# Performance work log

Hardware: AMD Instinct MI355X
Metric: run time of the kernel (lower is better)

Reference implementation:

```python
import jax, jax.numpy as jnp
import numpy as np

B, T, C = 8, 1024, 1024
H, D = 16, 64  # num_heads, head_size

def setup_inputs() -> dict:
    key = jax.random.key(0)
    ks = jax.random.split(key, 6)
    s = C ** -0.5
    return {
        "x": jax.random.normal(ks[0], (B, T, C), dtype=jnp.float32),
        "Wq": jax.random.normal(ks[1], (H, C, D), dtype=jnp.float32) * s,
        "Wk": jax.random.normal(ks[2], (H, C, D), dtype=jnp.float32) * s,
        "Wv": jax.random.normal(ks[3], (H, C, D), dtype=jnp.float32) * s,
        "Wproj": jax.random.normal(ks[4], (H * D, C), dtype=jnp.float32) * ((H * D) ** -0.5),
        "bproj": jnp.zeros((C,), dtype=jnp.float32),
    }

def reference(x, Wq, Wk, Wv, Wproj, bproj):
    # per-head QKV projections, batched over heads via einsum (same math as looped heads)
    q = jnp.einsum('btc,hcd->bhtd', x, Wq)
    k = jnp.einsum('btc,hcd->bhtd', x, Wk)
    v = jnp.einsum('btc,hcd->bhtd', x, Wv)
    scale = D ** -0.5  # k.shape[-1]**-0.5 in original head
    scores = jnp.einsum('bhtd,bhsd->bhts', q, k) * scale  # [B,H,T,T]
    Tn = x.shape[1]
    causal = jnp.tril(jnp.ones((Tn, Tn), dtype=bool))
    scores = jnp.where(causal, scores, jnp.float32(-jnp.inf))
    att = jax.nn.softmax(scores, axis=-1)
    out = jnp.einsum('bhts,bhsd->bhtd', att, v)          # [B,H,T,D]
    out = out.transpose(0, 2, 1, 3).reshape(x.shape[0], Tn, H * D)  # concat heads
    return out @ Wproj + bproj  # dropout is identity at p=0.0
```

## Files before the change

### kernel.cpp

```cpp
#include <hip/hip_runtime.h>
#include <hip/hip_bf16.h>

#define B_ 8
#define T_ 1024
#define C_ 1024
#define H_ 16
#define D_ 64
#define QKVLD 3072

typedef short v4s __attribute__((ext_vector_type(4)));
typedef short v8s __attribute__((ext_vector_type(8)));
typedef float v4f __attribute__((ext_vector_type(4)));
typedef float v16f __attribute__((ext_vector_type(16)));

__device__ __forceinline__ unsigned short f2b(float f) {
    unsigned int u = __builtin_bit_cast(unsigned int, f);
    unsigned int lsb = (u >> 16) & 1u;
    u += 0x7fffu + lsb;
    return (unsigned short)(u >> 16);
}

__device__ __forceinline__ float fexp2(float x) {
    return __expf(x * 0.69314718056f);
}

__device__ __forceinline__ v4s pack4(float p0, float p1, float p2, float p3) {
    unsigned int a = (__builtin_bit_cast(unsigned int, p0) + 0x8000u) >> 16;
    unsigned int b = (__builtin_bit_cast(unsigned int, p1) + 0x8000u) & 0xFFFF0000u;
    unsigned int c = (__builtin_bit_cast(unsigned int, p2) + 0x8000u) >> 16;
    unsigned int d = (__builtin_bit_cast(unsigned int, p3) + 0x8000u) & 0xFFFF0000u;
    union { unsigned int u[2]; v4s v; } t;
    t.u[0] = a | b; t.u[1] = c | d;
    return t.v;
}

#define MFMA32(A, B, C) __builtin_amdgcn_mfma_f32_16x16x32_bf16(A, B, C, 0, 0, 0)
#define MFMA16(A, B, C) __builtin_amdgcn_mfma_f32_16x16x16bf16_1k(A, B, C, 0, 0, 0)

#define GLOAD16(gp, lp)                                                          \
    __builtin_amdgcn_global_load_lds(                                            \
        (const __attribute__((address_space(1))) unsigned int*)(gp),             \
        (__attribute__((address_space(3))) unsigned int*)(lp), 16, 0, 0)

__global__ void prep_kernel(const float* __restrict__ x, const float* __restrict__ Wq,
                            const float* __restrict__ Wk, const float* __restrict__ Wv,
                            const float* __restrict__ Wproj,
                            unsigned short* __restrict__ xb,
                            unsigned short* __restrict__ WqkvT,
                            unsigned short* __restrict__ WprojT) {
    __shared__ unsigned short t[64][65];
    int g = blockIdx.x;
    if (g < 8192) {
        int i = (g * 256 + (int)threadIdx.x) * 4;
        float4 v = *(const float4*)(x + i);
        ushort4 o;
        o.x = f2b(v.x); o.y = f2b(v.y); o.z = f2b(v.z); o.w = f2b(v.w);
        *(ushort4*)(xb + i) = o;
    } else if (g < 8192 + 768) {
        int idx = g - 8192;
        int z = idx >> 4;
        int h = z / 3, part = z % 3;
        const float* src = (part == 0 ? Wq : (part == 1 ? Wk : Wv)) + (size_t)h * C_ * D_;
        int c0 = (idx & 15) * 64;
        for (int i = threadIdx.x; i < 4096; i += 256) {
            int r = i >> 6, d = i & 63;
            t[d][r] = f2b(src[(size_t)(c0 + r) * D_ + d]);
        }
        __syncthreads();
        unsigned short* dst = WqkvT + (size_t)(h * 192 + part * 64) * C_;
        for (int i = threadIdx.x; i < 4096; i += 256) {
            int d = i >> 6, r = i & 63;
            dst[(size_t)d * C_ + c0 + r] = t[d][r];
        }
    } else {
        int idx = g - 8960;
        int n0 = (idx & 15) * 64, k0 = (idx >> 4) * 64;
        for (int i = threadIdx.x; i < 4096; i += 256) {
            int r = i >> 6, c = i & 63;
            t[c][r] = f2b(Wproj[(size_t)(k0 + r) * C_ + n0 + c]);
        }
        __syncthreads();
        for (int i = threadIdx.x; i < 4096; i += 256) {
            int n = i >> 6, k = i & 63;
            WprojT[(size_t)(n0 + n) * 1024 + k0 + k] = t[n][k];
        }
    }
}

__global__ __launch_bounds__(256, 2) void gemm_qkv(const unsigned short* __restrict__ A,
                                                   const unsigned short* __restrict__ Bt,
                                                   unsigned short* __restrict__ Cout,
                                                   int M, int N, int K) {
    __shared__ unsigned short lA[2][256 * 32];
    __shared__ unsigned short lB[2][128 * 32];
    int tid = threadIdx.x;
    int m0 = blockIdx.y * 256, n0 = blockIdx.x * 128;
    int lane = tid & 63, w = tid >> 6;
    int half = lane >> 5, l32 = lane & 31;
    int wm = w >> 1, wn = w & 1;

    const unsigned short* gA[4];
    int offA[4];
    #pragma unroll
    for (int j = 0; j < 4; j++) {
        int c = j * 256 + tid;
        int row = c >> 2;
        int col8 = ((c & 3) ^ ((row >> 1) & 3)) * 8;
        gA[j] = A + (size_t)(m0 + row) * K + col8;
        offA[j] = (j * 256 + w * 64) * 16;
    }
    const unsigned short* gB[2];
    int offB[2];
    #pragma unroll
    for (int j = 0; j < 2; j++) {
        int c = j * 256 + tid;
        int row = c >> 2;
        int col8 = ((c & 3) ^ ((row >> 1) & 3)) * 8;
        gB[j] = Bt + (size_t)(n0 + row) * K + col8;
        offB[j] = (j * 256 + w * 64) * 16;
    }

    int am[4], bn[2];
    #pragma unroll
    for (int mi = 0; mi < 4; mi++) am[mi] = wm * 128 + mi * 32 + l32;
    #pragma unroll
    for (int ni = 0; ni < 2; ni++) bn[ni] = wn * 64 + ni * 32 + l32;

    v16f acc[4][2];
    #pragma unroll
    for (int mi = 0; mi < 4; mi++)
        #pragma unroll
        for (int ni = 0; ni < 2; ni++)
            #pragma unroll
            for (int r = 0; r < 16; r++) acc[mi][ni][r] = 0.f;

    int ktiles = K >> 5;
    #pragma unroll
    for (int j = 0; j < 4; j++) GLOAD16(gA[j], (char*)&lA[0][0] + offA[j]);
    #pragma unroll
    for (int j = 0; j < 2; j++) GLOAD16(gB[j], (char*)&lB[0][0] + offB[j]);

    for (int it = 0; it < ktiles; it++) {
        int cur = it & 1, nxt = cur ^ 1;
        __asm__ volatile("s_waitcnt vmcnt(0)" ::: "memory");
        __asm__ volatile("s_barrier" ::: "memory");
        {
            int kn = (it + 1 < ktiles) ? (it + 1) * 32 : it * 32;
            #pragma unroll
            for (int j = 0; j < 4; j++) GLOAD16(gA[j] + kn, (char*)&lA[nxt][0] + offA[j]);
            #pragma unroll
            for (int j = 0; j < 2; j++) GLOAD16(gB[j] + kn, (char*)&lB[nxt][0] + offB[j]);
        }
        #pragma unroll
        for (int step = 0; step < 2; step++) {
            int g = step * 2 + half;
            v8s af[4], bf[2];
            #pragma unroll
            for (int mi = 0; mi < 4; mi++)
                af[mi] = *(const v8s*)&lA[cur][am[mi] * 32 + ((g ^ ((am[mi] >> 1) & 3)) * 8)];
            #pragma unroll
            for (int ni = 0; ni < 2; ni++)
                bf[ni] = *(const v8s*)&lB[cur][bn[ni] * 32 + ((g ^ ((bn[ni] >> 1) & 3)) * 8)];
            #pragma unroll
            for (int mi = 0; mi < 4; mi++)
                #pragma unroll
                for (int ni = 0; ni < 2; ni++)
                    acc[mi][ni] = __builtin_amdgcn_mfma_f32_32x32x16_bf16(af[mi], bf[ni], acc[mi][ni], 0, 0, 0);
        }
    }
    #pragma unroll
    for (int mi = 0; mi < 4; mi++) {
        #pragma unroll
        for (int ni = 0; ni < 2; ni++) {
            int col = n0 + wn * 64 + ni * 32 + l32;
            #pragma unroll
            for (int r = 0; r < 16; r++) {
                int row = m0 + wm * 128 + mi * 32 + (r & 3) + 8 * (r >> 2) + 4 * half;
                Cout[(size_t)row * N + col] = f2b(acc[mi][ni][r]);
            }
        }
    }
}

__global__ __launch_bounds__(256, 3) void gemm_proj(const unsigned short* __restrict__ A,
                                                    const unsigned short* __restrict__ Bt,
                                                    float* __restrict__ Cout,
                                                    const float* __restrict__ bias,
                                                    int M, int N, int K) {
    constexpr int ABUF = 128 * 32;
    constexpr int BBUF = 128 * 32;
    __shared__ unsigned short lA[3 * ABUF];
    __shared__ unsigned short lB[3 * BBUF];

    int tid = threadIdx.x;
    int lane = tid & 63, w = tid >> 6;
    int half = lane >> 5, l32 = lane & 31;
    int wm = w >> 1, wn = w & 1;

    int g = blockIdx.x;
    int nbm = M / 128;
    int stripe = nbm >> 3;
    int xcd = g & 7, s = g >> 3;
    int m0 = (xcd * stripe + (s % stripe)) * 128;
    int n0 = (s / stripe) * 128;

    const unsigned short* gA[2];
    int offA[2];
    #pragma unroll
    for (int j = 0; j < 2; j++) {
        int c = j * 256 + tid;
        int row = c >> 2;
        int col8 = ((c & 3) ^ ((row >> 1) & 3)) * 8;
        gA[j] = A + (size_t)(m0 + row) * K + col8;
        offA[j] = (j * 256 + w * 64) * 16;
    }
    const unsigned short* gB[2];
    int offB[2];
    #pragma unroll
    for (int j = 0; j < 2; j++) {
        int c = j * 256 + tid;
        int row = c >> 2;
        int col8 = ((c & 3) ^ ((row >> 1) & 3)) * 8;
        gB[j] = Bt + (size_t)(n0 + row) * K + col8;
        offB[j] = (j * 256 + w * 64) * 16;
    }

    int am[2], bn[2];
    #pragma unroll
    for (int mi = 0; mi < 2; mi++) am[mi] = wm * 64 + mi * 32 + l32;
    #pragma unroll
    for (int ni = 0; ni < 2; ni++) bn[ni] = wn * 64 + ni * 32 + l32;

    v16f acc[2][2];
    #pragma unroll
    for (int mi = 0; mi < 2; mi++)
        #pragma unroll
        for (int ni = 0; ni < 2; ni++)
            #pragma unroll
            for (int r = 0; r < 16; r++) acc[mi][ni][r] = 0.f;

    int kt = K >> 5;
    #pragma unroll
    for (int j = 0; j < 2; j++) GLOAD16(gA[j], (char*)lA + offA[j]);
    #pragma unroll
    for (int j = 0; j < 2; j++) GLOAD16(gB[j], (char*)lB + offB[j]);
    #pragma unroll
    for (int j = 0; j < 2; j++) GLOAD16(gA[j] + 32, (char*)(lA + ABUF) + offA[j]);
    #pragma unroll
    for (int j = 0; j < 2; j++) GLOAD16(gB[j] + 32, (char*)(lB + BBUF) + offB[j]);

    int cur = 0;
    for (int it = 0; it < kt; it++) {
        int nx2 = cur + 2; if (nx2 >= 3) nx2 -= 3;
        __asm__ volatile("s_waitcnt vmcnt(4)" ::: "memory");
        __asm__ volatile("s_barrier" ::: "memory");
        {
            int kn = ((it + 2 < kt) ? it + 2 : kt - 1) << 5;
            #pragma unroll
            for (int j = 0; j < 2; j++) GLOAD16(gA[j] + kn, (char*)(lA + nx2 * ABUF) + offA[j]);
            #pragma unroll
            for (int j = 0; j < 2; j++) GLOAD16(gB[j] + kn, (char*)(lB + nx2 * BBUF) + offB[j]);
        }
        const unsigned short* bufA = lA + cur * ABUF;
        const unsigned short* bufB = lB + cur * BBUF;
        #pragma unroll
        for (int step = 0; step < 2; step++) {
            int gch = step * 2 + half;
            v8s af[2], bf[2];
            #pragma unroll
            for (int mi = 0; mi < 2; mi++)
                af[mi] = *(const v8s*)&bufA[am[mi] * 32 + ((gch ^ ((am[mi] >> 1) & 3)) * 8)];
            #pragma unroll
            for (int ni = 0; ni < 2; ni++)
                bf[ni] = *(const v8s*)&bufB[bn[ni] * 32 + ((gch ^ ((bn[ni] >> 1) & 3)) * 8)];
            #pragma unroll
            for (int mi = 0; mi < 2; mi++)
                #pragma unroll
                for (int ni = 0; ni < 2; ni++)
                    acc[mi][ni] = __builtin_amdgcn_mfma_f32_32x32x16_bf16(af[mi], bf[ni], acc[mi][ni], 0, 0, 0);
        }
        cur = cur + 1; if (cur >= 3) cur -= 3;
    }
    #pragma unroll
    for (int mi = 0; mi < 2; mi++) {
        #pragma unroll
        for (int ni = 0; ni < 2; ni++) {
            int col = n0 + wn * 64 + ni * 32 + l32;
            #pragma unroll
            for (int r = 0; r < 16; r++) {
                int row = m0 + wm * 64 + mi * 32 + (r & 3) + 8 * (r >> 2) + 4 * half;
                Cout[(size_t)row * N + col] = acc[mi][ni][r] + bias[col];
            }
        }
    }
}

__global__ void transpose_v(const unsigned short* __restrict__ QKV, unsigned short* __restrict__ Vt) {
    int t0 = blockIdx.x * 64;
    int bh = blockIdx.y;
    int b = bh >> 4, h = bh & 15;
    __shared__ unsigned short t[64][65];
    for (int i = threadIdx.x; i < 4096; i += 256) {
        int r = i >> 6, d = i & 63;
        t[d][r] = QKV[(size_t)(b * T_ + t0 + r) * QKVLD + h * 192 + 128 + d];
    }
    __syncthreads();
    for (int i = threadIdx.x; i < 4096; i += 256) {
        int d = i >> 6, r = i & 63;
        Vt[((size_t)bh * 64 + d) * T_ + t0 + r] = t[d][r];
    }
}

__global__ __launch_bounds__(256) void attn_kernel(const unsigned short* __restrict__ QKV,
                                                   const unsigned short* __restrict__ Vt,
                                                   unsigned short* __restrict__ Ob) {
    int bh = blockIdx.x;
    int qt = 7 - blockIdx.y;
    int b = bh >> 4, h = bh & 15;
    int tid = threadIdx.x, lane = tid & 63, w = tid >> 6;
    int quad = lane >> 4, l16 = lane & 15;
    int qg0 = qt * 128 + w * 32;

    __shared__ unsigned short lK[2][2][64][32];
    __shared__ unsigned short lV[2][64][32];

    v8s aq[2][2];
    #pragma unroll
    for (int st = 0; st < 2; st++) {
        const unsigned short* qp = QKV + (size_t)(b * T_ + qg0 + st * 16 + l16) * QKVLD + h * 192;
        aq[st][0] = *(const v8s*)(qp + quad * 8);
        aq[st][1] = *(const v8s*)(qp + 32 + quad * 8);
    }

    const unsigned short* gK[2];
    const unsigned short* gV[2];
    int ldsOff[2];
    #pragma unroll
    for (int j = 0; j < 2; j++) {
        int c = j * 256 + tid;
        int halfp = c >> 8, row = (c >> 2) & 63;
        int col8 = ((c & 3) ^ ((row >> 1) & 3)) * 8;
        gK[j] = QKV + (size_t)(b * T_ + row) * QKVLD + h * 192 + 64 + halfp * 32 + col8;
        gV[j] = Vt + ((size_t)bh * 64 + row) * T_ + halfp * 32 + col8;
        ldsOff[j] = (j * 256 + w * 64) * 16;
    }
    int rcol = (quad ^ ((l16 >> 1) & 3)) * 8;

    v4f accO[2][4];
    float lsum[2] = {0.f, 0.f};
    #pragma unroll
    for (int st = 0; st < 2; st++)
        #pragma unroll
        for (int i = 0; i < 4; i++) accO[st][i] = (v4f){0.f, 0.f, 0.f, 0.f};

    int ntiles = 2 * qt + 2;
    const float SC = 0.1803368801f;

    #pragma unroll
    for (int j = 0; j < 2; j++)
        GLOAD16(gK[j], (char*)&lK[0][0][0][0] + ldsOff[j]);

    for (int it = 0; it < ntiles; it++) {
        int cur = it & 1, nxt = cur ^ 1;
        int s0 = it * 64;
        __asm__ volatile("s_waitcnt vmcnt(0)" ::: "memory");
        __asm__ volatile("s_barrier" ::: "memory");
        #pragma unroll
        for (int j = 0; j < 2; j++)
            GLOAD16(gV[j] + s0, (char*)&lV[0][0][0] + ldsOff[j]);
        __asm__ volatile("" ::: "memory");
        {
            int itn = (it + 1 < ntiles) ? it + 1 : it;
            size_t koff = (size_t)itn * 64 * QKVLD;
            #pragma unroll
            for (int j = 0; j < 2; j++)
                GLOAD16(gK[j] + koff, (char*)&lK[nxt][0][0][0] + ldsOff[j]);
        }
        bool act0 = (qg0 + 15 >= s0);
        bool act1 = (qg0 + 31 >= s0);
        v4s pP[2][4];
        if (act1) {
            v4f sf[2][4];
            #pragma unroll
            for (int nt = 0; nt < 4; nt++) {
                v8s bk0 = *(const v8s*)&lK[cur][0][nt * 16 + l16][rcol];
                v8s bk1 = *(const v8s*)&lK[cur][1][nt * 16 + l16][rcol];
                v4f a1 = (v4f){0.f, 0.f, 0.f, 0.f};
                a1 = MFMA32(bk0, aq[1][0], a1);
                a1 = MFMA32(bk1, aq[1][1], a1);
                sf[1][nt] = a1;
                if (act0) {
                    v4f a0 = (v4f){0.f, 0.f, 0.f, 0.f};
                    a0 = MFMA32(bk0, aq[0][0], a0);
                    a0 = MFMA32(bk1, aq[0][1], a0);
                    sf[0][nt] = a0;
                }
            }
            bool diag = (it >= ntiles - 2);
            #pragma unroll
            for (int st = 0; st < 2; st++) {
                if (st == 0 && !act0) continue;
                int qg = qg0 + st * 16 + l16;
                #pragma unroll
                for (int nt = 0; nt < 4; nt++) {
                    float p[4];
                    #pragma unroll
                    for (int r = 0; r < 4; r++) {
                        if (diag) {
                            int sg = s0 + nt * 16 + quad * 4 + r;
                            p[r] = (sg > qg) ? 0.f : fexp2(sf[st][nt][r] * SC);
                        } else {
                            p[r] = fexp2(sf[st][nt][r] * SC);
                        }
                        lsum[st] += p[r];
                    }
                    pP[st][nt] = pack4(p[0], p[1], p[2], p[3]);
                }
            }
        }
        __asm__ volatile("s_waitcnt vmcnt(2)" ::: "memory");
        __asm__ volatile("s_barrier" ::: "memory");
        if (act1) {
            #pragma unroll
            for (int kb = 0; kb < 4; kb++) {
                int sc_ = kb >> 1;
                int ccg = (kb & 1) * 2 + (quad >> 1);
                #pragma unroll
                for (int dt = 0; dt < 4; dt++) {
                    int d = dt * 16 + l16;
                    int ccp = ccg ^ ((l16 >> 1) & 3);
                    v4s bv = *(const v4s*)&lV[sc_][d][ccp * 8 + (quad & 1) * 4];
                    accO[1][dt] = MFMA16(pP[1][kb], bv, accO[1][dt]);
                    if (act0) accO[0][dt] = MFMA16(pP[0][kb], bv, accO[0][dt]);
                }
            }
        }
    }
    #pragma unroll
    for (int st = 0; st < 2; st++) {
        float ls = lsum[st];
        ls += __shfl_xor(ls, 16, 64);
        ls += __shfl_xor(ls, 32, 64);
        #pragma unroll
        for (int r = 0; r < 4; r++) {
            float lq = __shfl(ls, quad * 4 + r, 64);
            float inv = 1.0f / lq;
            int q = qg0 + st * 16 + quad * 4 + r;
            #pragma unroll
            for (int dt = 0; dt < 4; dt++) {
                int d = dt * 16 + l16;
                Ob[(size_t)(b * T_ + q) * (H_ * D_) + h * 64 + d] = f2b(accO[st][dt][r] * inv);
            }
        }
    }
}

extern "C" void kernel_launch(void* const* d_in, const int* in_sizes, int n_in,
                              void* d_out, int out_size, void* d_ws, size_t ws_size,
                              hipStream_t stream) {
    const float* x     = (const float*)d_in[0];
    const float* Wq    = (const float*)d_in[1];
    const float* Wk    = (const float*)d_in[2];
    const float* Wv    = (const float*)d_in[3];
    const float* Wproj = (const float*)d_in[4];
    const float* bproj = (const float*)d_in[5];
    float* out = (float*)d_out;

    char* ws = (char*)d_ws;
    unsigned short* xb     = (unsigned short*)ws;
    unsigned short* WqkvT  = (unsigned short*)(ws + 16777216);
    unsigned short* WprojT = (unsigned short*)(ws + 23068672);
    unsigned short* QKV    = (unsigned short*)(ws + 25165824);
    unsigned short* Vt     = (unsigned short*)(ws + 75497472);
    unsigned short* Ob     = (unsigned short*)(ws + 92274688);

    prep_kernel<<<dim3(9216), dim3(256), 0, stream>>>(x, Wq, Wk, Wv, Wproj, xb, WqkvT, WprojT);
    gemm_qkv<<<dim3(24, 32), dim3(256), 0, stream>>>(xb, WqkvT, QKV, 8192, 3072, 1024);
    transpose_v<<<dim3(16, 128), dim3(256), 0, stream>>>(QKV, Vt);
    attn_kernel<<<dim3(128, 8), dim3(256), 0, stream>>>(QKV, Vt, Ob);
    gemm_proj<<<dim3(512), dim3(256), 0, stream>>>(Ob, WprojT, out, bproj, 8192, 1024, 1024);
}
```

Before: 240.7 us.

## Enlarge QKV GEMM tile to 256x384 with 512 threads and triple-buffered LDS

```diff
diff --git a/kernel.cpp b/kernel.cpp
--- a/kernel.cpp
+++ b/kernel.cpp
@@ -87,92 +87,105 @@
     }
 }
 
-__global__ __launch_bounds__(256, 2) void gemm_qkv(const unsigned short* __restrict__ A,
+__global__ __launch_bounds__(512, 2) void gemm_qkv(const unsigned short* __restrict__ A,
                                                    const unsigned short* __restrict__ Bt,
                                                    unsigned short* __restrict__ Cout,
                                                    int M, int N, int K) {
-    __shared__ unsigned short lA[2][256 * 32];
-    __shared__ unsigned short lB[2][128 * 32];
+    constexpr int ABUF = 256 * 32;
+    constexpr int BBUF = 384 * 32;
+    __shared__ unsigned short lA[3 * ABUF];
+    __shared__ unsigned short lB[3 * BBUF];
     int tid = threadIdx.x;
-    int m0 = blockIdx.y * 256, n0 = blockIdx.x * 128;
     int lane = tid & 63, w = tid >> 6;
     int half = lane >> 5, l32 = lane & 31;
-    int wm = w >> 1, wn = w & 1;
-
-    const unsigned short* gA[4];
-    int offA[4];
-    #pragma unroll
-    for (int j = 0; j < 4; j++) {
-        int c = j * 256 + tid;
+    int wm = w >> 2, wn = w & 3;
+
+    int g = blockIdx.x;
+    int n0 = (g & 7) * 384;
+    int m0 = (g >> 3) * 256;
+
+    const unsigned short* gA[2];
+    int offA[2];
+    #pragma unroll
+    for (int j = 0; j < 2; j++) {
+        int c = j * 512 + tid;
         int row = c >> 2;
         int col8 = ((c & 3) ^ ((row >> 1) & 3)) * 8;
         gA[j] = A + (size_t)(m0 + row) * K + col8;
-        offA[j] = (j * 256 + w * 64) * 16;
-    }
-    const unsigned short* gB[2];
-    int offB[2];
-    #pragma unroll
-    for (int j = 0; j < 2; j++) {
-        int c = j * 256 + tid;
+        offA[j] = (j * 512 + w * 64) * 16;
+    }
+    const unsigned short* gB[3];
+    int offB[3];
+    #pragma unroll
+    for (int j = 0; j < 3; j++) {
+        int c = j * 512 + tid;
         int row = c >> 2;
         int col8 = ((c & 3) ^ ((row >> 1) & 3)) * 8;
         gB[j] = Bt + (size_t)(n0 + row) * K + col8;
-        offB[j] = (j * 256 + w * 64) * 16;
-    }
-
-    int am[4], bn[2];
+        offB[j] = (j * 512 + w * 64) * 16;
+    }
+
+    int am[4], bn[3];
     #pragma unroll
     for (int mi = 0; mi < 4; mi++) am[mi] = wm * 128 + mi * 32 + l32;
     #pragma unroll
-    for (int ni = 0; ni < 2; ni++) bn[ni] = wn * 64 + ni * 32 + l32;
-
-    v16f acc[4][2];
+    for (int ni = 0; ni < 3; ni++) bn[ni] = wn * 96 + ni * 32 + l32;
+
+    v16f acc[4][3];
     #pragma unroll
     for (int mi = 0; mi < 4; mi++)
         #pragma unroll
-        for (int ni = 0; ni < 2; ni++)
+        for (int ni = 0; ni < 3; ni++)
             #pragma unroll
             for (int r = 0; r < 16; r++) acc[mi][ni][r] = 0.f;
 
-    int ktiles = K >> 5;
-    #pragma unroll
-    for (int j = 0; j < 4; j++) GLOAD16(gA[j], (char*)&lA[0][0] + offA[j]);
-    #pragma unroll
-    for (int j = 0; j < 2; j++) GLOAD16(gB[j], (char*)&lB[0][0] + offB[j]);
-
-    for (int it = 0; it < ktiles; it++) {
-        int cur = it & 1, nxt = cur ^ 1;
-        __asm__ volatile("s_waitcnt vmcnt(0)" ::: "memory");
+    int kt = K >> 5;
+    #pragma unroll
+    for (int j = 0; j < 2; j++) GLOAD16(gA[j], (char*)lA + offA[j]);
+    #pragma unroll
+    for (int j = 0; j < 3; j++) GLOAD16(gB[j], (char*)lB + offB[j]);
+    #pragma unroll
+    for (int j = 0; j < 2; j++) GLOAD16(gA[j] + 32, (char*)(lA + ABUF) + offA[j]);
+    #pragma unroll
+    for (int j = 0; j < 3; j++) GLOAD16(gB[j] + 32, (char*)(lB + BBUF) + offB[j]);
+
+    int cur = 0;
+    for (int it = 0; it < kt; it++) {
+        int nx2 = cur + 2; if (nx2 >= 3) nx2 -= 3;
+        __asm__ volatile("s_waitcnt vmcnt(5)" ::: "memory");
         __asm__ volatile("s_barrier" ::: "memory");
         {
-            int kn = (it + 1 < ktiles) ? (it + 1) * 32 : it * 32;
-            #pragma unroll
-            for (int j = 0; j < 4; j++) GLOAD16(gA[j] + kn, (char*)&lA[nxt][0] + offA[j]);
-            #pragma unroll
-            for (int j = 0; j < 2; j++) GLOAD16(gB[j] + kn, (char*)&lB[nxt][0] + offB[j]);
-        }
+            int kn = ((it + 2 < kt) ? it + 2 : kt - 1) << 5;
+            #pragma unroll
+            for (int j = 0; j < 2; j++) GLOAD16(gA[j] + kn, (char*)(lA + nx2 * ABUF) + offA[j]);
+            #pragma unroll
+            for (int j = 0; j < 3; j++) GLOAD16(gB[j] + kn, (char*)(lB + nx2 * BBUF) + offB[j]);
+        }
+        const unsigned short* bufA = lA + cur * ABUF;
+        const unsigned short* bufB = lB + cur * BBUF;
         #pragma unroll
         for (int step = 0; step < 2; step++) {
-            int g = step * 2 + half;
-            v8s af[4], bf[2];
+            int gch = step * 2 + half;
+            v8s af[4], bf[3];
             #pragma unroll
             for (int mi = 0; mi < 4; mi++)
-                af[mi] = *(const v8s*)&lA[cur][am[mi] * 32 + ((g ^ ((am[mi] >> 1) & 3)) * 8)];
-            #pragma unroll
-            for (int ni = 0; ni < 2; ni++)
-                bf[ni] = *(const v8s*)&lB[cur][bn[ni] * 32 + ((g ^ ((bn[ni] >> 1) & 3)) * 8)];
+                af[mi] = *(const v8s*)&bufA[am[mi] * 32 + ((gch ^ ((am[mi] >> 1) & 3)) * 8)];
+            #pragma unroll
+            for (int ni = 0; ni < 3; ni++)
+                bf[ni] = *(const v8s*)&bufB[bn[ni] * 32 + ((gch ^ ((bn[ni] >> 1) & 3)) * 8)];
             #pragma unroll
             for (int mi = 0; mi < 4; mi++)
                 #pragma unroll
-                for (int ni = 0; ni < 2; ni++)
+                for (int ni = 0; ni < 3; ni++)
                     acc[mi][ni] = __builtin_amdgcn_mfma_f32_32x32x16_bf16(af[mi], bf[ni], acc[mi][ni], 0, 0, 0);
         }
+        cur = cur + 1; if (cur >= 3) cur -= 3;
     }
     #pragma unroll
     for (int mi = 0; mi < 4; mi++) {
         #pragma unroll
-        for (int ni = 0; ni < 2; ni++) {
-            int col = n0 + wn * 64 + ni * 32 + l32;
+        for (int ni = 0; ni < 3; ni++) {
+            int col = n0 + wn * 96 + ni * 32 + l32;
             #pragma unroll
             for (int r = 0; r < 16; r++) {
                 int row = m0 + wm * 128 + mi * 32 + (r & 3) + 8 * (r >> 2) + 4 * half;
@@ -475,7 +488,7 @@
     unsigned short* Ob     = (unsigned short*)(ws + 92274688);
 
     prep_kernel<<<dim3(9216), dim3(256), 0, stream>>>(x, Wq, Wk, Wv, Wproj, xb, WqkvT, WprojT);
-    gemm_qkv<<<dim3(24, 32), dim3(256), 0, stream>>>(xb, WqkvT, QKV, 8192, 3072, 1024);
+    gemm_qkv<<<dim3(256), dim3(512), 0, stream>>>(xb, WqkvT, QKV, 8192, 3072, 1024);
     transpose_v<<<dim3(16, 128), dim3(256), 0, stream>>>(QKV, Vt);
     attn_kernel<<<dim3(128, 8), dim3(256), 0, stream>>>(QKV, Vt, Ob);
     gemm_proj<<<dim3(512), dim3(256), 0, stream>>>(Ob, WprojT, out, bproj, 8192, 1024, 1024);
```

Result: no change. 241.8 us (+0.5%).

## Fuse V transpose into QKV GEMM epilogue and regroup weights by Q/K/V

Applied to the files above, without the earlier changes.

```diff
diff --git a/kernel.cpp b/kernel.cpp
--- a/kernel.cpp
+++ b/kernel.cpp
@@ -67,7 +67,7 @@
             t[d][r] = f2b(src[(size_t)(c0 + r) * D_ + d]);
         }
         __syncthreads();
-        unsigned short* dst = WqkvT + (size_t)(h * 192 + part * 64) * C_;
+        unsigned short* dst = WqkvT + (size_t)(part * 1024 + h * 64) * C_;
         for (int i = threadIdx.x; i < 4096; i += 256) {
             int d = i >> 6, r = i & 63;
             dst[(size_t)d * C_ + c0 + r] = t[d][r];
@@ -90,9 +90,14 @@
 __global__ __launch_bounds__(256, 2) void gemm_qkv(const unsigned short* __restrict__ A,
                                                    const unsigned short* __restrict__ Bt,
                                                    unsigned short* __restrict__ Cout,
+                                                   unsigned short* __restrict__ Vt,
                                                    int M, int N, int K) {
-    __shared__ unsigned short lA[2][256 * 32];
-    __shared__ unsigned short lB[2][128 * 32];
+    constexpr int ABUF = 256 * 32;
+    constexpr int BBUF = 128 * 32;
+    __shared__ unsigned short smem[2 * ABUF + 2 * BBUF];
+    unsigned short* lA0 = smem;
+    unsigned short* lB0 = smem + 2 * ABUF;
+
     int tid = threadIdx.x;
     int m0 = blockIdx.y * 256, n0 = blockIdx.x * 128;
     int lane = tid & 63, w = tid >> 6;
@@ -136,9 +141,9 @@
 
     int ktiles = K >> 5;
     #pragma unroll
-    for (int j = 0; j < 4; j++) GLOAD16(gA[j], (char*)&lA[0][0] + offA[j]);
-    #pragma unroll
-    for (int j = 0; j < 2; j++) GLOAD16(gB[j], (char*)&lB[0][0] + offB[j]);
+    for (int j = 0; j < 4; j++) GLOAD16(gA[j], (char*)lA0 + offA[j]);
+    #pragma unroll
+    for (int j = 0; j < 2; j++) GLOAD16(gB[j], (char*)lB0 + offB[j]);
 
     for (int it = 0; it < ktiles; it++) {
         int cur = it & 1, nxt = cur ^ 1;
@@ -147,20 +152,22 @@
         {
             int kn = (it + 1 < ktiles) ? (it + 1) * 32 : it * 32;
             #pragma unroll
-            for (int j = 0; j < 4; j++) GLOAD16(gA[j] + kn, (char*)&lA[nxt][0] + offA[j]);
-            #pragma unroll
-            for (int j = 0; j < 2; j++) GLOAD16(gB[j] + kn, (char*)&lB[nxt][0] + offB[j]);
-        }
+            for (int j = 0; j < 4; j++) GLOAD16(gA[j] + kn, (char*)(lA0 + nxt * ABUF) + offA[j]);
+            #pragma unroll
+            for (int j = 0; j < 2; j++) GLOAD16(gB[j] + kn, (char*)(lB0 + nxt * BBUF) + offB[j]);
+        }
+        const unsigned short* bufA = lA0 + cur * ABUF;
+        const unsigned short* bufB = lB0 + cur * BBUF;
         #pragma unroll
         for (int step = 0; step < 2; step++) {
             int g = step * 2 + half;
             v8s af[4], bf[2];
             #pragma unroll
             for (int mi = 0; mi < 4; mi++)
-                af[mi] = *(const v8s*)&lA[cur][am[mi] * 32 + ((g ^ ((am[mi] >> 1) & 3)) * 8)];
+                af[mi] = *(const v8s*)&bufA[am[mi] * 32 + ((g ^ ((am[mi] >> 1) & 3)) * 8)];
             #pragma unroll
             for (int ni = 0; ni < 2; ni++)
-                bf[ni] = *(const v8s*)&lB[cur][bn[ni] * 32 + ((g ^ ((bn[ni] >> 1) & 3)) * 8)];
+                bf[ni] = *(const v8s*)&bufB[bn[ni] * 32 + ((g ^ ((bn[ni] >> 1) & 3)) * 8)];
             #pragma unroll
             for (int mi = 0; mi < 4; mi++)
                 #pragma unroll
@@ -168,15 +175,48 @@
                     acc[mi][ni] = __builtin_amdgcn_mfma_f32_32x32x16_bf16(af[mi], bf[ni], acc[mi][ni], 0, 0, 0);
         }
     }
-    #pragma unroll
-    for (int mi = 0; mi < 4; mi++) {
-        #pragma unroll
-        for (int ni = 0; ni < 2; ni++) {
-            int col = n0 + wn * 64 + ni * 32 + l32;
-            #pragma unroll
-            for (int r = 0; r < 16; r++) {
-                int row = m0 + wm * 128 + mi * 32 + (r & 3) + 8 * (r >> 2) + 4 * half;
-                Cout[(size_t)row * N + col] = f2b(acc[mi][ni][r]);
+    if (n0 < 2048) {
+        #pragma unroll
+        for (int mi = 0; mi < 4; mi++) {
+            #pragma unroll
+            for (int ni = 0; ni < 2; ni++) {
+                int col = n0 + wn * 64 + ni * 32 + l32;
+                #pragma unroll
+                for (int r = 0; r < 16; r++) {
+                    int row = m0 + wm * 128 + mi * 32 + (r & 3) + 8 * (r >> 2) + 4 * half;
+                    Cout[(size_t)row * N + col] = f2b(acc[mi][ni][r]);
+                }
+            }
+        }
+    } else {
+        unsigned short* sT = smem;
+        int bB = m0 >> 10;
+        int t0 = m0 & 1023;
+        #pragma unroll
+        for (int p = 0; p < 2; p++) {
+            __syncthreads();
+            if (wn == p) {
+                #pragma unroll
+                for (int mi = 0; mi < 4; mi++)
+                    #pragma unroll
+                    for (int ni = 0; ni < 2; ni++) {
+                        int cl = ni * 32 + l32;
+                        #pragma unroll
+                        for (int r = 0; r < 16; r++) {
+                            int rowl = wm * 128 + mi * 32 + (r & 3) + 8 * (r >> 2) + 4 * half;
+                            sT[cl * 258 + rowl] = f2b(acc[mi][ni][r]);
+                        }
+                    }
+            }
+            __syncthreads();
+            #pragma unroll
+            for (int j = 0; j < 8; j++) {
+                int c = j * 256 + tid;
+                int rw = c >> 5, ch = c & 31;
+                int vcol = (n0 - 2048) + p * 64 + rw;
+                int hh = vcol >> 6, dd = vcol & 63;
+                *(v8s*)&Vt[(((size_t)bB * 16 + hh) * 64 + dd) * T_ + t0 + ch * 8] =
+                    *(const v8s*)&sT[rw * 258 + ch * 8];
             }
         }
     }
@@ -295,22 +335,6 @@
     }
 }
 
-__global__ void transpose_v(const unsigned short* __restrict__ QKV, unsigned short* __restrict__ Vt) {
-    int t0 = blockIdx.x * 64;
-    int bh = blockIdx.y;
-    int b = bh >> 4, h = bh & 15;
-    __shared__ unsigned short t[64][65];
-    for (int i = threadIdx.x; i < 4096; i += 256) {
-        int r = i >> 6, d = i & 63;
-        t[d][r] = QKV[(size_t)(b * T_ + t0 + r) * QKVLD + h * 192 + 128 + d];
-    }
-    __syncthreads();
-    for (int i = threadIdx.x; i < 4096; i += 256) {
-        int d = i >> 6, r = i & 63;
-        Vt[((size_t)bh * 64 + d) * T_ + t0 + r] = t[d][r];
-    }
-}
-
 __global__ __launch_bounds__(256) void attn_kernel(const unsigned short* __restrict__ QKV,
                                                    const unsigned short* __restrict__ Vt,
                                                    unsigned short* __restrict__ Ob) {
@@ -327,7 +351,7 @@
     v8s aq[2][2];
     #pragma unroll
     for (int st = 0; st < 2; st++) {
-        const unsigned short* qp = QKV + (size_t)(b * T_ + qg0 + st * 16 + l16) * QKVLD + h * 192;
+        const unsigned short* qp = QKV + (size_t)(b * T_ + qg0 + st * 16 + l16) * QKVLD + h * 64;
         aq[st][0] = *(const v8s*)(qp + quad * 8);
         aq[st][1] = *(const v8s*)(qp + 32 + quad * 8);
     }
@@ -340,7 +364,7 @@
         int c = j * 256 + tid;
         int halfp = c >> 8, row = (c >> 2) & 63;
         int col8 = ((c & 3) ^ ((row >> 1) & 3)) * 8;
-        gK[j] = QKV + (size_t)(b * T_ + row) * QKVLD + h * 192 + 64 + halfp * 32 + col8;
+        gK[j] = QKV + (size_t)(b * T_ + row) * QKVLD + 1024 + h * 64 + halfp * 32 + col8;
         gV[j] = Vt + ((size_t)bh * 64 + row) * T_ + halfp * 32 + col8;
         ldsOff[j] = (j * 256 + w * 64) * 16;
     }
@@ -475,8 +499,7 @@
     unsigned short* Ob     = (unsigned short*)(ws + 92274688);
 
     prep_kernel<<<dim3(9216), dim3(256), 0, stream>>>(x, Wq, Wk, Wv, Wproj, xb, WqkvT, WprojT);
-    gemm_qkv<<<dim3(24, 32), dim3(256), 0, stream>>>(xb, WqkvT, QKV, 8192, 3072, 1024);
-    transpose_v<<<dim3(16, 128), dim3(256), 0, stream>>>(QKV, Vt);
+    gemm_qkv<<<dim3(24, 32), dim3(256), 0, stream>>>(xb, WqkvT, QKV, Vt, 8192, 3072, 1024);
     attn_kernel<<<dim3(128, 8), dim3(256), 0, stream>>>(QKV, Vt, Ob);
     gemm_proj<<<dim3(512), dim3(256), 0, stream>>>(Ob, WprojT, out, bproj, 8192, 1024, 1024);
 }
```

After: 240.7 us. About the same (+0.0%).
